# Performance work log

Measured on AMD Instinct MI355X. Metric: run time of the kernel, lower is better.

## Reference

```python
import jax, jax.numpy as jnp
import numpy as np

B, L, E, H, ENC, V, NL = 64, 512, 128, 512, 256, 4, 2
SOS = 4


def setup_inputs() -> dict:
    key = jax.random.key(0)
    ks = jax.random.split(key, 20)
    s = 0.05
    r = lambda k, shp: (jax.random.normal(k, shp, jnp.float32) * s)
    return {
        "encoder_outputs": jax.random.normal(ks[0], (B, L, ENC), jnp.float32),
        "targets": jax.random.randint(ks[1], (B, L), 0, V),
        "encoder_mask": jnp.ones((B, L), bool),
        "teacher_forcing_ratio": 1,
        "emb": r(ks[2], (V + 2, E)),
        "Wh": r(ks[3], (H, H)),
        "Ws": r(ks[4], (H, ENC)),
        "v": r(ks[5], (1, H)),
        "Wih0": r(ks[6], (3 * H, E + ENC)),
        "Whh0": r(ks[7], (3 * H, H)),
        "bih0": r(ks[8], (3 * H,)),
        "bhh0": r(ks[9], (3 * H,)),
        "Wih1": r(ks[10], (3 * H, H)),
        "Whh1": r(ks[11], (3 * H, H)),
        "bih1": r(ks[12], (3 * H,)),
        "bhh1": r(ks[13], (3 * H,)),
        "Wout": r(ks[14], (V, H)),
        "bout": r(ks[15], (V,)),
        "Winit": r(ks[16], (H * NL, ENC)),
        "binit": r(ks[17], (H * NL,)),
    }


def gru_cell(x, h, Wih, Whh, bih, bhh):
    # PyTorch GRUCell math
    gi = x @ Wih.T + bih
    gh = h @ Whh.T + bhh
    ir, iz, inn = jnp.split(gi, 3, axis=-1)
    hr, hz, hn = jnp.split(gh, 3, axis=-1)
    rg = jax.nn.sigmoid(ir + hr)
    zg = jax.nn.sigmoid(iz + hz)
    ng = jnp.tanh(inn + rg * hn)
    return (1.0 - zg) * ng + zg * h


def reference(encoder_outputs, targets, encoder_mask, teacher_forcing_ratio,
              emb, Wh, Ws, v, Wih0, Whh0, bih0, bhh0, Wih1, Whh1, bih1, bhh1,
              Wout, bout, Winit, binit):
    # init hidden: masked mean-pool -> linear -> tanh, (NL, B, H)
    maskf = encoder_mask[..., None].astype(jnp.float32)
    pooled = (encoder_outputs * maskf).sum(1) / jnp.clip(maskf.sum(1), 1.0)
    h0 = jnp.tanh((pooled @ Winit.T + binit).reshape(B, NL, H).transpose(1, 0, 2))

    # attention keys precomputed once (same linear applied each step in torch)
    keys = jnp.einsum('ble,he->blh', encoder_outputs, Ws)  # (B, L, H)

    # teacher forcing ratio fixed at 1 -> inputs known ahead of time
    tokens = jnp.concatenate([jnp.full((B, 1), SOS, targets.dtype), targets[:, :-1]], axis=1)
    emb_seq = emb[tokens]  # (B, L, E)

    neg = jnp.finfo(jnp.float32).min

    def step(h, e_t):
        q = h[-1] @ Wh.T                                   # (B, H)
        energy = jnp.tanh(q[:, None, :] + keys)            # (B, L, H)
        scores = jnp.einsum('blh,h->bl', energy, v[0])     # (B, L)
        scores = jnp.where(encoder_mask, scores, neg)
        attn = jax.nn.softmax(scores, axis=-1)
        ctx = jnp.einsum('bl,ble->be', attn, encoder_outputs)
        x = jnp.concatenate([e_t, ctx], axis=-1)           # (B, E+ENC)
        h0n = gru_cell(x, h[0], Wih0, Whh0, bih0, bhh0)
        h1n = gru_cell(h0n, h[1], Wih1, Whh1, bih1, bhh1)
        logits = h1n @ Wout.T + bout                       # (B, V)
        return jnp.stack([h0n, h1n]), logits

    _, logits = jax.lax.scan(step, h0, emb_seq.transpose(1, 0, 2))
    return logits.transpose(1, 0, 2)  # (B, L, V)
```

## Files before the change

### kernel.cpp

```cpp
#include <hip/hip_runtime.h>
#include <cstdint>
#include <cstddef>


#define BB   64
#define LL   512
#define EE   128
#define HH   512
#define ED   256
#define VV   4
#define SOS  4

#define NBLK 512
#define NTHR 256

typedef unsigned short ushort8 __attribute__((ext_vector_type(8)));
typedef unsigned int uint;
typedef uint  uint4v  __attribute__((ext_vector_type(4)));
typedef float float4v __attribute__((ext_vector_type(4)));

static const size_t OFF_KEYS = 0;
static const size_t OFF_WH   = 33554432;
static const size_t OFF_WHH0 = 34078720;
static const size_t OFF_WIH1 = 35651584;
static const size_t OFF_WHH1 = 37224448;
static const size_t OFF_WIHC = 38797312;
static const size_t OFF_GTOK = 39583744;
static const size_t OFF_H0   = 39620608;
static const size_t OFF_H1   = 39751680;
static const size_t OFF_QQ   = 39882752;
static const size_t OFF_CTXP = 40407040;
static const size_t OFF_SS   = 40931328;
static const size_t OFF_H0Q  = 40933376;
static const size_t OFF_H1Q  = 40998912;
static const size_t OFF_FLG  = 41064448;
static const size_t OFF_CNT  = 41097216;
static const size_t OFF_LP   = 41097728;

#define L_KEYS 0
#define L_H0F  65536
#define L_H1F  66560
#define L_QB   67584
#define L_VV   69696
#define L_CTX  71808
#define L_SCB  72832
#define L_ATB  73088
#define L_RED  73344
#define L_PRED 73408
#define L_GH0  77504
#define L_GH1  78272
#define L_H0O  79040
#define L_H1O  79296
#define L_TOT  79552

#define UC_LD4(dst, ptr) \
  asm volatile("global_load_dwordx4 %0, %1, off sc0 sc1" : "=v"(dst) : "v"(ptr))
#define UC_ST4(ptr, v4) \
  asm volatile("global_store_dwordx4 %0, %1, off sc0 sc1" :: "v"(ptr), "v"(v4) : "memory")
#define UC_FENCE() \
  do { asm volatile("s_waitcnt vmcnt(0)" ::: "memory"); \
       __builtin_amdgcn_sched_barrier(0); } while (0)

__device__ __forceinline__ float bfu(unsigned short u) {
  return __uint_as_float(((unsigned)u) << 16);
}
__device__ __forceinline__ float bflo(uint u) { return __uint_as_float(u << 16); }
__device__ __forceinline__ float bfhi(uint u) { return __uint_as_float(u & 0xffff0000u); }
__device__ __forceinline__ unsigned short f2bf(float f) {
  unsigned u = __float_as_uint(f);
  unsigned r = 0x7FFFu + ((u >> 16) & 1u);
  return (unsigned short)((u + r) >> 16);
}
__device__ __forceinline__ uint packbf(float a, float b) {
  return (uint)f2bf(a) | ((uint)f2bf(b) << 16);
}
__device__ __forceinline__ float tanh_fast(float x) {
  x = __builtin_amdgcn_fmed3f(x, -10.f, 10.f);
  float t = __builtin_amdgcn_exp2f(x * 2.8853900817779268f);
  return (t - 1.f) * __builtin_amdgcn_rcpf(t + 1.f);
}
__device__ __forceinline__ float sigmoid_fast(float x) {
  x = __builtin_amdgcn_fmed3f(x, -30.f, 30.f);
  float t = __builtin_amdgcn_exp2f(x * -1.4426950408889634f);
  return __builtin_amdgcn_rcpf(1.f + t);
}
__device__ __forceinline__ float exp_fast(float x) {
  return __builtin_amdgcn_exp2f(x * 1.4426950408889634f);
}
__device__ __forceinline__ float gloadf(const float* p) {
  return __hip_atomic_load(p, __ATOMIC_RELAXED, __HIP_MEMORY_SCOPE_AGENT);
}
__device__ __forceinline__ void gstoref(float* p, float v) {
  __hip_atomic_store(p, v, __ATOMIC_RELAXED, __HIP_MEMORY_SCOPE_AGENT);
}
__device__ __forceinline__ uint gloadu(const uint* p) {
  return __hip_atomic_load(p, __ATOMIC_RELAXED, __HIP_MEMORY_SCOPE_AGENT);
}
__device__ __forceinline__ void gstoreu(uint* p, uint v) {
  __hip_atomic_store(p, v, __ATOMIC_RELAXED, __HIP_MEMORY_SCOPE_AGENT);
}

__device__ __forceinline__ void octet_sync(char* ws, int b, int j, uint gen) {
  asm volatile("s_waitcnt vmcnt(0)" ::: "memory");
  __syncthreads();
  const int tid = threadIdx.x;
  uint* fl = (uint*)(ws + OFF_FLG);
  if (tid == 0)
    gstoreu(fl + (size_t)(b * 8 + j) * 16, gen);
  if (tid < 8 && tid != j) {
    while (gloadu(fl + (size_t)(b * 8 + tid) * 16) < gen)
      __builtin_amdgcn_s_sleep(4);
  }
  __syncthreads();
}


__global__ void k_prep(const float* Wh, const float* Whh0, const float* Wih0,
                       const float* Wih1, const float* Whh1, char* ws) {
  unsigned short* Whbf   = (unsigned short*)(ws + OFF_WH);
  unsigned short* Whh0bf = (unsigned short*)(ws + OFF_WHH0);
  unsigned short* Wih1bf = (unsigned short*)(ws + OFF_WIH1);
  unsigned short* Whh1bf = (unsigned short*)(ws + OFF_WHH1);
  unsigned short* WihCbf = (unsigned short*)(ws + OFF_WIHC);
  const int tot = 262144 + 786432 * 3 + 393216;
  for (int i = blockIdx.x * blockDim.x + threadIdx.x; i < tot; i += gridDim.x * blockDim.x) {
    if (i < 262144) { Whbf[i] = f2bf(Wh[i]); }
    else if (i < 262144 + 786432) { int jj = i - 262144; Whh0bf[jj] = f2bf(Whh0[jj]); }
    else if (i < 262144 + 2 * 786432) { int jj = i - 262144 - 786432; Wih1bf[jj] = f2bf(Wih1[jj]); }
    else if (i < 262144 + 3 * 786432) { int jj = i - 262144 - 2 * 786432; Whh1bf[jj] = f2bf(Whh1[jj]); }
    else {
      int jj = i - 262144 - 3 * 786432;
      int r = jj >> 8, e = jj & 255;
      WihCbf[jj] = f2bf(Wih0[(size_t)r * 384 + 128 + e]);
    }
  }
}

__global__ void k_gitok(const float* emb, const float* Wih0, const float* bih0, char* ws) {
  float* gt = (float*)(ws + OFF_GTOK);
  const int vt = blockIdx.x;
  const int tid = threadIdx.x;
  __shared__ float ev[EE];
  if (tid < EE) ev[tid] = emb[(size_t)vt * EE + tid];
  __syncthreads();
  for (int r = tid; r < 1536; r += 256) {
    float a = bih0[r];
    const float* wr = Wih0 + (size_t)r * 384;
    for (int e = 0; e < EE; ++e) a += wr[e] * ev[e];
    gt[(size_t)vt * 1536 + r] = a;
  }
}

__global__ void k_keys(const float* enc, const float* Ws, char* ws) {
  unsigned short* keys = (unsigned short*)(ws + OFF_KEYS);
  __shared__ float et[32][ED];
  const int tid = threadIdx.x;
  const int row0 = blockIdx.x * 32;
  for (int r = 0; r < 32; ++r) et[r][tid] = enc[(size_t)(row0 + r) * ED + tid];
  __syncthreads();
  for (int hhh = 0; hhh < 2; ++hhh) {
    const int h = hhh * 256 + tid;
    float acc[32];
    #pragma unroll
    for (int ll = 0; ll < 32; ++ll) acc[ll] = 0.f;
    const float4* wrow = (const float4*)(Ws + (size_t)h * ED);
    for (int e4 = 0; e4 < 64; ++e4) {
      float4 w = wrow[e4];
      #pragma unroll
      for (int ll = 0; ll < 32; ++ll) {
        acc[ll] += w.x * et[ll][e4 * 4] + w.y * et[ll][e4 * 4 + 1]
                 + w.z * et[ll][e4 * 4 + 2] + w.w * et[ll][e4 * 4 + 3];
      }
    }
    for (int ll = 0; ll < 32; ++ll)
      keys[(size_t)(row0 + ll) * HH + h] = f2bf(acc[ll]);
  }
}

__global__ void k_init(const float* enc, const float* Winit, const float* binit, char* ws) {
  const int b = blockIdx.x;
  const int tid = threadIdx.x;
  __shared__ float pooled[ED];
  float acc = 0.f;
  for (int l = 0; l < LL; ++l) acc += enc[((size_t)b * LL + l) * ED + tid];
  pooled[tid] = acc * (1.0f / 512.0f);
  __syncthreads();
  float* h0 = (float*)(ws + OFF_H0);
  float* h1 = (float*)(ws + OFF_H1);
  for (int pass = 0; pass < 4; ++pass) {
    const int jj = pass * 256 + tid;
    float a = binit[jj];
    const float* wr = Winit + (size_t)jj * ED;
    for (int e = 0; e < ED; ++e) a += wr[e] * pooled[e];
    const float val = tanh_fast(a);
    const int nl = jj >> 9, h = jj & 511;
    if (nl == 0) h0[(size_t)b * HH + h] = val;
    else h1[(size_t)b * HH + h] = val;
  }
  if (b == 0) {
    uint* fl = (uint*)(ws + OFF_FLG);
    for (int i = tid; i < 8192; i += 256) fl[i] = 0u;
    uint* cnt = (uint*)(ws + OFF_CNT);
    if (tid < 128) cnt[tid] = 0u;
  }
}

__launch_bounds__(NTHR, 2)
__global__ void k_decode(char* ws, const float* enc, const int* targets,
                         const float* vvec, const float* bhh0, const float* bhh1,
                         const float* bih1, const float* Wout) {
  extern __shared__ char smem[];
  const int tid = threadIdx.x;

  __shared__ int roleSh[2];
  if (tid == 0) {
    uint xcd;
    asm volatile("s_getreg_b32 %0, hwreg(HW_REG_XCC_ID)" : "=s"(xcd));
    xcd &= 7u;
    uint* cnt = (uint*)(ws + OFF_CNT);
    uint rank = __hip_atomic_fetch_add(cnt + (size_t)xcd * 16, 1u,
                                       __ATOMIC_RELAXED, __HIP_MEMORY_SCOPE_AGENT);
    roleSh[0] = (int)(rank & 63);
    roleSh[1] = (int)xcd;
  }
  __syncthreads();
  const int b = roleSh[0], j = roleSh[1];

  const unsigned short* keysg  = (const unsigned short*)(ws + OFF_KEYS);
  const unsigned short* Whbf   = (const unsigned short*)(ws + OFF_WH);
  const unsigned short* Whh0bf = (const unsigned short*)(ws + OFF_WHH0);
  const unsigned short* Wih1bf = (const unsigned short*)(ws + OFF_WIH1);
  const unsigned short* Whh1bf = (const unsigned short*)(ws + OFF_WHH1);
  const unsigned short* WihCbf = (const unsigned short*)(ws + OFF_WIHC);
  const float* gi_tok = (const float*)(ws + OFF_GTOK);

  uint*  QQg   = (uint*)(ws + OFF_QQ)   + (size_t)b * 2048;
  float* CTXPg = (float*)(ws + OFF_CTXP) + (size_t)b * 2048;
  float* SSg   = (float*)(ws + OFF_SS)  + (size_t)b * 8;
  uint*  H0Qg  = (uint*)(ws + OFF_H0Q)  + (size_t)b * 256;
  uint*  H1Qg  = (uint*)(ws + OFF_H1Q)  + (size_t)b * 256;
  float* lp    = (float*)(ws + OFF_LP);

  uint*  h0u   = (uint*)(smem + L_H0F);
  uint*  h1u   = (uint*)(smem + L_H1F);
  float* qbf   = (float*)(smem + L_QB);
  float* vvf   = (float*)(smem + L_VV);
  float* ctx   = (float*)(smem + L_CTX);
  float* scb   = (float*)(smem + L_SCB);
  float* atb   = (float*)(smem + L_ATB);
  float* wred  = (float*)(smem + L_RED);
  float* pRed  = (float*)(smem + L_PRED);
  float* gh0own = (float*)(smem + L_GH0);
  float* gh1own = (float*)(smem + L_GH1);
  float* h0own = (float*)(smem + L_H0O);
  float* h1own = (float*)(smem + L_H1O);
  uint*  qstage = (uint*)(smem + L_PRED);
  uint*  hstage = (uint*)(smem + L_SCB);

  for (int c = tid; c < 4096; c += NTHR) {
    const int l = c >> 6, hs = c & 63;
    ushort8 kv = *(const ushort8*)(keysg + ((size_t)(b * LL + j * 64 + l) * HH + hs * 8));
    *(ushort8*)(smem + L_KEYS + l * 1024 + ((hs * 16) ^ ((l & 7) << 4))) = kv;
  }
  for (int h = tid; h < 512; h += NTHR)
    vvf[(h >> 7) * 132 + (h & 127)] = vvec[h];
  {
    const float* H0g = (const float*)(ws + OFF_H0) + (size_t)b * HH;
    const float* H1g = (const float*)(ws + OFF_H1) + (size_t)b * HH;
    h0u[tid] = packbf(H0g[2 * tid], H0g[2 * tid + 1]);
    h1u[tid] = packbf(H1g[2 * tid], H1g[2 * tid + 1]);
    if (tid < 64) {
      h0own[tid] = H0g[j * 64 + tid];
      h1own[tid] = H1g[j * 64 + tid];
    }
  }
  uint encp[32];
  {
    const float* ebase = enc + ((size_t)(b * LL + j * 64)) * ED + tid;
    #pragma unroll
    for (int k = 0; k < 32; ++k)
      encp[k] = packbf(ebase[(size_t)(2 * k) * ED], ebase[(size_t)(2 * k + 1) * ED]);
  }
  uint whq[64];
  #pragma unroll
  for (int i = 0; i < 32; ++i) {
    whq[i]      = *(const uint*)(Whbf + (size_t)(2 * tid) * HH + j * 64 + 2 * i);
    whq[32 + i] = *(const uint*)(Whbf + (size_t)(2 * tid + 1) * HH + j * 64 + 2 * i);
  }
  __syncthreads();

  {
    float q0 = 0.f, q1 = 0.f;
    #pragma unroll
    for (int i = 0; i < 32; ++i) {
      const float hl = h1own[2 * i], hh = h1own[2 * i + 1];
      q0 += bflo(whq[i]) * hl + bfhi(whq[i]) * hh;
      q1 += bflo(whq[32 + i]) * hl + bfhi(whq[32 + i]) * hh;
    }
    qstage[tid] = packbf(q0, q1);
    if (tid < 32) hstage[tid] = packbf(h1own[2 * tid], h1own[2 * tid + 1]);
    __syncthreads();
    if (tid < 64) { UC_ST4(QQg + (size_t)j * 256 + 4 * tid, *(uint4v*)(qstage + 4 * tid)); }
    else if (tid < 72) {
      const int c = tid - 64;
      UC_ST4(H1Qg + (size_t)j * 32 + 4 * c, *(uint4v*)(hstage + 4 * c));
    }
  }
  octet_sync(ws, b, j, 1u);

  for (int t = 0; t < LL; ++t) {
    if (tid < 64) {
      uint4v uq0, uq1, uq2, uq3, uq4, uq5, uq6, uq7;
      UC_LD4(uq0, QQg + 0 * 256 + 4 * tid);
      UC_LD4(uq1, QQg + 1 * 256 + 4 * tid);
      UC_LD4(uq2, QQg + 2 * 256 + 4 * tid);
      UC_LD4(uq3, QQg + 3 * 256 + 4 * tid);
      UC_LD4(uq4, QQg + 4 * 256 + 4 * tid);
      UC_LD4(uq5, QQg + 5 * 256 + 4 * tid);
      UC_LD4(uq6, QQg + 6 * 256 + 4 * tid);
      UC_LD4(uq7, QQg + 7 * 256 + 4 * tid);
      UC_FENCE();
      const int base = ((8 * tid) >> 7) * 132 + ((8 * tid) & 127);
      #pragma unroll
      for (int k = 0; k < 4; ++k) {
        float lo = bflo(uq0[k]) + bflo(uq1[k]) + bflo(uq2[k]) + bflo(uq3[k])
                 + bflo(uq4[k]) + bflo(uq5[k]) + bflo(uq6[k]) + bflo(uq7[k]);
        float hi = bfhi(uq0[k]) + bfhi(uq1[k]) + bfhi(uq2[k]) + bfhi(uq3[k])
                 + bfhi(uq4[k]) + bfhi(uq5[k]) + bfhi(uq6[k]) + bfhi(uq7[k]);
        qbf[base + 2 * k]     = lo;
        qbf[base + 2 * k + 1] = hi;
      }
    } else if (tid < 120) {
      const int p2 = (tid - 64) >> 3, c = (tid - 64) & 7;
      const int p = p2 + (p2 >= j);
      uint4v u;
      UC_LD4(u, H1Qg + (size_t)p * 32 + 4 * c);
      UC_FENCE();
      *(uint4v*)(h1u + p * 32 + 4 * c) = u;
    }
    __syncthreads();

    {
      const int mat = tid >> 7, seg = (tid >> 6) & 1, r = tid & 63;
      const unsigned short* W = mat ? Whh1bf : Whh0bf;
      const uint* hsrc = (mat ? h1u : h0u) + seg * 128;
      const ushort8* w0 = (const ushort8*)(W + (size_t)(0 * 512 + j * 64 + r) * 512 + seg * 256);
      const ushort8* w1 = (const ushort8*)(W + (size_t)(1 * 512 + j * 64 + r) * 512 + seg * 256);
      const ushort8* w2 = (const ushort8*)(W + (size_t)(2 * 512 + j * 64 + r) * 512 + seg * 256);
      float a0 = 0.f, a1 = 0.f, a2 = 0.f;
      for (int k8 = 0; k8 < 32; ++k8) {
        const uint4 hu = *(const uint4*)(hsrc + k8 * 4);
        const ushort8 u0 = w0[k8], u1 = w1[k8], u2 = w2[k8];
        float hv[8];
        hv[0] = bflo(hu.x); hv[1] = bfhi(hu.x); hv[2] = bflo(hu.y); hv[3] = bfhi(hu.y);
        hv[4] = bflo(hu.z); hv[5] = bfhi(hu.z); hv[6] = bflo(hu.w); hv[7] = bfhi(hu.w);
        #pragma unroll
        for (int u = 0; u < 8; ++u) {
          a0 += bfu(u0[u]) * hv[u];
          a1 += bfu(u1[u]) * hv[u];
          a2 += bfu(u2[u]) * hv[u];
        }
      }
      pRed[((mat * 2 + seg) * 3 + 0) * 64 + r] = a0;
      pRed[((mat * 2 + seg) * 3 + 1) * 64 + r] = a1;
      pRed[((mat * 2 + seg) * 3 + 2) * 64 + r] = a2;
    }

    {
      const int lloc = tid >> 2, hq = tid & 3;
      const char* kbase = smem + L_KEYS + lloc * 1024;
      const int xo = (lloc & 7) << 4;
      const float* qh = qbf + hq * 132;
      const float* vh = vvf + hq * 132;
      float s = 0.f;
      for (int i8 = 0; i8 < 16; ++i8) {
        ushort8 kk = *(const ushort8*)(kbase + ((hq * 256 + i8 * 16) ^ xo));
        const float* q8 = qh + i8 * 8;
        const float* v8 = vh + i8 * 8;
        #pragma unroll
        for (int u = 0; u < 8; ++u)
          s += v8[u] * tanh_fast(q8[u] + bfu(kk[u]));
      }
      s += __shfl_xor(s, 1);
      s += __shfl_xor(s, 2);
      if (hq == 0) scb[lloc] = s;
    }
    __syncthreads();

    if (tid < 64) {
      float e = exp_fast(scb[tid]);
      atb[tid] = e;
      float s2 = e;
      #pragma unroll
      for (int off = 32; off >= 1; off >>= 1) s2 += __shfl_xor(s2, off);
      if (tid == 0) gstoref(SSg + j, s2);
    }
    __syncthreads();

    {
      float a = 0.f;
      #pragma unroll
      for (int k = 0; k < 32; ++k) {
        uint u = encp[k];
        a += atb[2 * k] * bflo(u) + atb[2 * k + 1] * bfhi(u);
      }
      ctx[tid] = a;
    }
    for (int o = tid; o < 384; o += NTHR) {
      const int m = (o >= 192) ? 1 : 0, oo = o - m * 192, g = oo >> 6, r = oo & 63;
      const float v = pRed[((m * 2 + 0) * 3 + g) * 64 + r]
                    + pRed[((m * 2 + 1) * 3 + g) * 64 + r]
                    + (m ? bhh1 : bhh0)[g * 512 + j * 64 + r];
      (m ? gh1own : gh0own)[g * 64 + r] = v;
    }
    __syncthreads();
    if (tid < 64) { UC_ST4((uint*)(CTXPg + (size_t)j * 256) + 4 * tid, *(uint4v*)((uint*)ctx + 4 * tid)); }
    octet_sync(ws, b, j, (uint)(3 * t + 2));

    {
      const int c = tid & 63, p0 = tid >> 6;
      float4v f0, f1;
      UC_LD4(f0, (const uint*)(CTXPg + (size_t)p0 * 256) + 4 * c);
      UC_LD4(f1, (const uint*)(CTXPg + (size_t)(p0 + 4) * 256) + 4 * c);
      float ssv = 0.f;
      if (tid < 8) ssv = gloadf(SSg + tid);
      UC_FENCE();
      if (tid < 8) wred[tid] = ssv;
      *(float4v*)(pRed + (size_t)p0 * 256 + 4 * c) = f0 + f1;
      __syncthreads();
      const float S8 = ((wred[0] + wred[1]) + (wred[2] + wred[3]))
                     + ((wred[4] + wred[5]) + (wred[6] + wred[7]));
      const float rS = __builtin_amdgcn_rcpf(S8);
      ctx[tid] = (pRed[0 * 256 + tid] + pRed[1 * 256 + tid]
                + pRed[2 * 256 + tid] + pRed[3 * 256 + tid]) * rS;
    }
    __syncthreads();
    {
      const int r = tid & 63, q4 = tid >> 6;
      const ushort8* w0 = (const ushort8*)(WihCbf + (size_t)(0 * 512 + j * 64 + r) * 256 + q4 * 64);
      const ushort8* w1 = (const ushort8*)(WihCbf + (size_t)(1 * 512 + j * 64 + r) * 256 + q4 * 64);
      const ushort8* w2 = (const ushort8*)(WihCbf + (size_t)(2 * 512 + j * 64 + r) * 256 + q4 * 64);
      const float* cx = ctx + q4 * 64;
      float a0 = 0.f, a1 = 0.f, a2 = 0.f;
      for (int k8 = 0; k8 < 8; ++k8) {
        const ushort8 u0 = w0[k8], u1 = w1[k8], u2 = w2[k8];
        #pragma unroll
        for (int u = 0; u < 8; ++u) {
          const float c = cx[k8 * 8 + u];
          a0 += bfu(u0[u]) * c; a1 += bfu(u1[u]) * c; a2 += bfu(u2[u]) * c;
        }
      }
      pRed[(q4 * 3 + 0) * 64 + r] = a0;
      pRed[(q4 * 3 + 1) * 64 + r] = a1;
      pRed[(q4 * 3 + 2) * 64 + r] = a2;
    }
    __syncthreads();
    if (tid < 64) {
      const int r = tid;
      const int tok = (t == 0) ? SOS : targets[(size_t)b * LL + t - 1];
      const float* gt = gi_tok + (size_t)tok * 1536 + j * 64 + r;
      const float g0 = pRed[(0 * 3 + 0) * 64 + r] + pRed[(1 * 3 + 0) * 64 + r]
                     + pRed[(2 * 3 + 0) * 64 + r] + pRed[(3 * 3 + 0) * 64 + r] + gt[0];
      const float g1 = pRed[(0 * 3 + 1) * 64 + r] + pRed[(1 * 3 + 1) * 64 + r]
                     + pRed[(2 * 3 + 1) * 64 + r] + pRed[(3 * 3 + 1) * 64 + r] + gt[512];
      const float g2 = pRed[(0 * 3 + 2) * 64 + r] + pRed[(1 * 3 + 2) * 64 + r]
                     + pRed[(2 * 3 + 2) * 64 + r] + pRed[(3 * 3 + 2) * 64 + r] + gt[1024];
      const float rg = sigmoid_fast(g0 + gh0own[r]);
      const float zg = sigmoid_fast(g1 + gh0own[64 + r]);
      const float ng = tanh_fast(g2 + rg * gh0own[128 + r]);
      h0own[r] = (1.f - zg) * ng + zg * h0own[r];
    }
    __syncthreads();
    if (tid < 32) {
      const uint pk = packbf(h0own[2 * tid], h0own[2 * tid + 1]);
      h0u[j * 32 + tid] = pk;
      hstage[tid] = pk;
    }
    __syncthreads();
    if (tid < 8) { UC_ST4(H0Qg + (size_t)j * 32 + 4 * tid, *(uint4v*)(hstage + 4 * tid)); }
    octet_sync(ws, b, j, (uint)(3 * t + 3));

    if (tid < 56) {
      const int p2 = tid >> 3, c = tid & 7;
      const int p = p2 + (p2 >= j);
      uint4v u;
      UC_LD4(u, H0Qg + (size_t)p * 32 + 4 * c);
      UC_FENCE();
      *(uint4v*)(h0u + p * 32 + 4 * c) = u;
    }
    __syncthreads();
    {
      const int r = tid & 63, s4 = tid >> 6;
      const ushort8* w0 = (const ushort8*)(Wih1bf + (size_t)(0 * 512 + j * 64 + r) * 512 + s4 * 128);
      const ushort8* w1 = (const ushort8*)(Wih1bf + (size_t)(1 * 512 + j * 64 + r) * 512 + s4 * 128);
      const ushort8* w2 = (const ushort8*)(Wih1bf + (size_t)(2 * 512 + j * 64 + r) * 512 + s4 * 128);
      const uint* hsrc = h0u + s4 * 64;
      float a0 = 0.f, a1 = 0.f, a2 = 0.f;
      for (int k8 = 0; k8 < 16; ++k8) {
        const uint4 hu = *(const uint4*)(hsrc + k8 * 4);
        const ushort8 u0 = w0[k8], u1 = w1[k8], u2 = w2[k8];
        float hv[8];
        hv[0] = bflo(hu.x); hv[1] = bfhi(hu.x); hv[2] = bflo(hu.y); hv[3] = bfhi(hu.y);
        hv[4] = bflo(hu.z); hv[5] = bfhi(hu.z); hv[6] = bflo(hu.w); hv[7] = bfhi(hu.w);
        #pragma unroll
        for (int u = 0; u < 8; ++u) {
          a0 += bfu(u0[u]) * hv[u];
          a1 += bfu(u1[u]) * hv[u];
          a2 += bfu(u2[u]) * hv[u];
        }
      }
      pRed[(s4 * 3 + 0) * 64 + r] = a0;
      pRed[(s4 * 3 + 1) * 64 + r] = a1;
      pRed[(s4 * 3 + 2) * 64 + r] = a2;
    }
    __syncthreads();
    if (tid < 64) {
      const int r = tid;
      const float g0 = pRed[(0 * 3 + 0) * 64 + r] + pRed[(1 * 3 + 0) * 64 + r]
                     + pRed[(2 * 3 + 0) * 64 + r] + pRed[(3 * 3 + 0) * 64 + r]
                     + bih1[0 * 512 + j * 64 + r];
      const float g1 = pRed[(0 * 3 + 1) * 64 + r] + pRed[(1 * 3 + 1) * 64 + r]
                     + pRed[(2 * 3 + 1) * 64 + r] + pRed[(3 * 3 + 1) * 64 + r]
                     + bih1[1 * 512 + j * 64 + r];
      const float g2 = pRed[(0 * 3 + 2) * 64 + r] + pRed[(1 * 3 + 2) * 64 + r]
                     + pRed[(2 * 3 + 2) * 64 + r] + pRed[(3 * 3 + 2) * 64 + r]
                     + bih1[2 * 512 + j * 64 + r];
      const float rg = sigmoid_fast(g0 + gh1own[r]);
      const float zg = sigmoid_fast(g1 + gh1own[64 + r]);
      const float ng = tanh_fast(g2 + rg * gh1own[128 + r]);
      h1own[r] = (1.f - zg) * ng + zg * h1own[r];
    }
    __syncthreads();
    {
      float q0 = 0.f, q1 = 0.f;
      #pragma unroll
      for (int i = 0; i < 32; ++i) {
        const float hl = h1own[2 * i], hh = h1own[2 * i + 1];
        q0 += bflo(whq[i]) * hl + bfhi(whq[i]) * hh;
        q1 += bflo(whq[32 + i]) * hl + bfhi(whq[32 + i]) * hh;
      }
      qstage[tid] = packbf(q0, q1);
    }
    if (tid < 32) {
      const uint pk = packbf(h1own[2 * tid], h1own[2 * tid + 1]);
      h1u[j * 32 + tid] = pk;
      hstage[tid] = pk;
    }
    if (tid >= 64 && tid < 128) {
      const int lane = tid - 64, v = lane >> 4, i = lane & 15;
      float a = 0.f;
      #pragma unroll
      for (int k = 0; k < 4; ++k)
        a += Wout[(size_t)v * HH + j * 64 + i * 4 + k] * h1own[i * 4 + k];
      a += __shfl_xor(a, 8); a += __shfl_xor(a, 4);
      a += __shfl_xor(a, 2); a += __shfl_xor(a, 1);
      if (i == 0) lp[(((size_t)t * BB + b) * 8 + j) * 4 + v] = a;
    }
    __syncthreads();
    if (tid < 64) { UC_ST4(QQg + (size_t)j * 256 + 4 * tid, *(uint4v*)(qstage + 4 * tid)); }
    else if (tid < 72) {
      const int c = tid - 64;
      UC_ST4(H1Qg + (size_t)j * 32 + 4 * c, *(uint4v*)(hstage + 4 * c));
    }
    octet_sync(ws, b, j, (uint)(3 * t + 4));
  }
}

__global__ void k_lsum(const char* ws, const float* bout, float* out) {
  const float* lp = (const float*)(ws + OFF_LP);
  const int i = blockIdx.x * 256 + threadIdx.x;
  if (i >= BB * LL * VV) return;
  const int v = i & 3, t = (i >> 2) & 511, b = i >> 11;
  float a = bout[v];
  #pragma unroll
  for (int jj = 0; jj < 8; ++jj)
    a += lp[(((size_t)t * BB + b) * 8 + jj) * 4 + v];
  out[i] = a;
}

extern "C" void kernel_launch(void* const* d_in, const int* in_sizes, int n_in,
                              void* d_out, int out_size, void* d_ws, size_t ws_size,
                              hipStream_t stream) {
  char* ws = (char*)d_ws;
  const float* enc     = (const float*)d_in[0];
  const int*   targets = (const int*)d_in[1];
  const float* emb   = (const float*)d_in[4];
  const float* Wh    = (const float*)d_in[5];
  const float* Ws    = (const float*)d_in[6];
  const float* vvec  = (const float*)d_in[7];
  const float* Wih0  = (const float*)d_in[8];
  const float* Whh0  = (const float*)d_in[9];
  const float* bih0  = (const float*)d_in[10];
  const float* bhh0  = (const float*)d_in[11];
  const float* Wih1  = (const float*)d_in[12];
  const float* Whh1  = (const float*)d_in[13];
  const float* bih1  = (const float*)d_in[14];
  const float* bhh1  = (const float*)d_in[15];
  const float* Wout  = (const float*)d_in[16];
  const float* bout  = (const float*)d_in[17];
  const float* Winit = (const float*)d_in[18];
  const float* binit = (const float*)d_in[19];

  k_prep <<<1024, 256, 0, stream>>>(Wh, Whh0, Wih0, Wih1, Whh1, ws);
  k_gitok<<<6,    256, 0, stream>>>(emb, Wih0, bih0, ws);
  k_keys <<<1024, 256, 0, stream>>>(enc, Ws, ws);
  k_init <<<64,   256, 0, stream>>>(enc, Winit, binit, ws);

  (void)hipFuncSetAttribute((const void*)k_decode,
                            hipFuncAttributeMaxDynamicSharedMemorySize, L_TOT);

  {
    void* kws = (void*)ws;
    void* ken = (void*)enc;
    void* ktg = (void*)targets;
    void* kvv = (void*)vvec;
    void* kb0 = (void*)bhh0;
    void* kb1 = (void*)bhh1;
    void* kbi = (void*)bih1;
    void* kwo = (void*)Wout;
    void* args[] = { &kws, &ken, &ktg, &kvv, &kb0, &kb1, &kbi, &kwo };
    hipError_t ce = hipLaunchCooperativeKernel((const void*)k_decode, dim3(NBLK), dim3(NTHR),
                                               args, L_TOT, stream);
    if (ce != hipSuccess) {
      k_decode<<<dim3(NBLK), dim3(NTHR), L_TOT, stream>>>(ws, enc, targets, vvec,
                                                          bhh0, bhh1, bih1, Wout);
    }
  }

  k_lsum<<<512, 256, 0, stream>>>(ws, bout, (float*)d_out);
}
```

Baseline: 49.45 ms.

## Process two batch rows per block with split publish/wait syncs and fp16 dot2 GEMVs

Halves the grid so each persistent block owns two batch rows. It interleaves their per-step phases so one row's cross-block wait can overlap the other row's compute. The octet barrier is split into separate publish and wait halves. The GRU weight matrices and hidden-state packing switch from bf16 to fp16 so the matvecs can use the fdot2 instruction. This trades occupancy and much larger shared memory (two key tiles) for fewer idle barrier waits, and fp16 weights bring some range and precision risk.

```diff
diff --git a/kernel.cpp b/kernel.cpp
--- a/kernel.cpp
+++ b/kernel.cpp
@@ -11,13 +11,14 @@
 #define VV   4
 #define SOS  4
 
-#define NBLK 512
+#define NBLK 256
 #define NTHR 256
 
 typedef unsigned short ushort8 __attribute__((ext_vector_type(8)));
 typedef unsigned int uint;
 typedef uint  uint4v  __attribute__((ext_vector_type(4)));
 typedef float float4v __attribute__((ext_vector_type(4)));
+typedef _Float16 h2v __attribute__((ext_vector_type(2)));
 
 static const size_t OFF_KEYS = 0;
 static const size_t OFF_WH   = 33554432;
@@ -37,21 +38,24 @@
 static const size_t OFF_CNT  = 41097216;
 static const size_t OFF_LP   = 41097728;
 
-#define L_KEYS 0
-#define L_H0F  65536
-#define L_H1F  66560
-#define L_QB   67584
-#define L_VV   69696
-#define L_CTX  71808
-#define L_SCB  72832
-#define L_ATB  73088
-#define L_RED  73344
-#define L_PRED 73408
-#define L_GH0  77504
-#define L_GH1  78272
-#define L_H0O  79040
-#define L_H1O  79296
-#define L_TOT  79552
+#define LKEY(bi)  ((bi) * 65536)
+#define LB(bi)    (131072 + (bi) * 12544)
+#define O_H0U  0
+#define O_H1U  1024
+#define O_QBF  2048
+#define O_CTX  4160
+#define O_SCB  5184
+#define O_ATB  5440
+#define O_WRED 5696
+#define O_PRED 5760
+#define O_GH0  9856
+#define O_GH1  10624
+#define O_H0O  11392
+#define O_H1O  11648
+#define O_HST  11904
+#define O_CTXH 12032
+#define L_VV   156160
+#define L_TOT  158272
 
 #define UC_LD4(dst, ptr) \
   asm volatile("global_load_dwordx4 %0, %1, off sc0 sc1" : "=v"(dst) : "v"(ptr))
@@ -74,6 +78,24 @@
 __device__ __forceinline__ uint packbf(float a, float b) {
   return (uint)f2bf(a) | ((uint)f2bf(b) << 16);
 }
+__device__ __forceinline__ unsigned short f2h(float f) {
+  return __builtin_bit_cast(unsigned short, (_Float16)f);
+}
+__device__ __forceinline__ uint packh(float a, float b) {
+  return (uint)f2h(a) | ((uint)f2h(b) << 16);
+}
+__device__ __forceinline__ float fd2(uint w, uint h, float acc) {
+#if __has_builtin(__builtin_amdgcn_fdot2)
+  return __builtin_amdgcn_fdot2(__builtin_bit_cast(h2v, w),
+                                __builtin_bit_cast(h2v, h), acc, false);
+#else
+  acc += (float)__builtin_bit_cast(_Float16, (unsigned short)(w & 0xffffu)) *
+         (float)__builtin_bit_cast(_Float16, (unsigned short)(h & 0xffffu));
+  acc += (float)__builtin_bit_cast(_Float16, (unsigned short)(w >> 16)) *
+         (float)__builtin_bit_cast(_Float16, (unsigned short)(h >> 16));
+  return acc;
+#endif
+}
 __device__ __forceinline__ float tanh_fast(float x) {
   x = __builtin_amdgcn_fmed3f(x, -10.f, 10.f);
   float t = __builtin_amdgcn_exp2f(x * 2.8853900817779268f);
@@ -100,16 +122,16 @@
   __hip_atomic_store(p, v, __ATOMIC_RELAXED, __HIP_MEMORY_SCOPE_AGENT);
 }
 
-__device__ __forceinline__ void octet_sync(char* ws, int b, int j, uint gen) {
+__device__ __forceinline__ void oct_publish(char* ws, int b, int j, uint gen) {
   asm volatile("s_waitcnt vmcnt(0)" ::: "memory");
   __syncthreads();
-  const int tid = threadIdx.x;
-  uint* fl = (uint*)(ws + OFF_FLG);
-  if (tid == 0)
-    gstoreu(fl + (size_t)(b * 8 + j) * 16, gen);
-  if (tid < 8 && tid != j) {
-    while (gloadu(fl + (size_t)(b * 8 + tid) * 16) < gen)
-      __builtin_amdgcn_s_sleep(4);
+  if (threadIdx.x == 0)
+    gstoreu((uint*)(ws + OFF_FLG) + (size_t)(b * 8 + j) * 16, gen);
+}
+__device__ __forceinline__ void oct_wait(char* ws, int b, uint gen) {
+  if (threadIdx.x < 8) {
+    const uint* fp = (const uint*)(ws + OFF_FLG) + (size_t)(b * 8 + threadIdx.x) * 16;
+    while (gloadu(fp) < gen) __builtin_amdgcn_s_sleep(1);
   }
   __syncthreads();
 }
@@ -117,21 +139,21 @@
 
 __global__ void k_prep(const float* Wh, const float* Whh0, const float* Wih0,
                        const float* Wih1, const float* Whh1, char* ws) {
-  unsigned short* Whbf   = (unsigned short*)(ws + OFF_WH);
-  unsigned short* Whh0bf = (unsigned short*)(ws + OFF_WHH0);
-  unsigned short* Wih1bf = (unsigned short*)(ws + OFF_WIH1);
-  unsigned short* Whh1bf = (unsigned short*)(ws + OFF_WHH1);
-  unsigned short* WihCbf = (unsigned short*)(ws + OFF_WIHC);
+  unsigned short* Whbf  = (unsigned short*)(ws + OFF_WH);
+  unsigned short* W0F   = (unsigned short*)(ws + OFF_WHH0);
+  unsigned short* Wi1F  = (unsigned short*)(ws + OFF_WIH1);
+  unsigned short* W1F   = (unsigned short*)(ws + OFF_WHH1);
+  unsigned short* WicF  = (unsigned short*)(ws + OFF_WIHC);
   const int tot = 262144 + 786432 * 3 + 393216;
   for (int i = blockIdx.x * blockDim.x + threadIdx.x; i < tot; i += gridDim.x * blockDim.x) {
     if (i < 262144) { Whbf[i] = f2bf(Wh[i]); }
-    else if (i < 262144 + 786432) { int jj = i - 262144; Whh0bf[jj] = f2bf(Whh0[jj]); }
-    else if (i < 262144 + 2 * 786432) { int jj = i - 262144 - 786432; Wih1bf[jj] = f2bf(Wih1[jj]); }
-    else if (i < 262144 + 3 * 786432) { int jj = i - 262144 - 2 * 786432; Whh1bf[jj] = f2bf(Whh1[jj]); }
+    else if (i < 262144 + 786432) { int jj = i - 262144; W0F[jj] = f2h(Whh0[jj]); }
+    else if (i < 262144 + 2 * 786432) { int jj = i - 262144 - 786432; Wi1F[jj] = f2h(Wih1[jj]); }
+    else if (i < 262144 + 3 * 786432) { int jj = i - 262144 - 2 * 786432; W1F[jj] = f2h(Whh1[jj]); }
     else {
       int jj = i - 262144 - 3 * 786432;
       int r = jj >> 8, e = jj & 255;
-      WihCbf[jj] = f2bf(Wih0[(size_t)r * 384 + 128 + e]);
+      WicF[jj] = f2h(Wih0[(size_t)r * 384 + 128 + e]);
     }
   }
 }
@@ -205,7 +227,7 @@
   }
 }
 
-__launch_bounds__(NTHR, 2)
+__launch_bounds__(NTHR, 1)
 __global__ void k_decode(char* ws, const float* enc, const int* targets,
                          const float* vvec, const float* bhh0, const float* bhh1,
                          const float* bih1, const float* Wout) {
@@ -220,315 +242,63 @@
     uint* cnt = (uint*)(ws + OFF_CNT);
     uint rank = __hip_atomic_fetch_add(cnt + (size_t)xcd * 16, 1u,
                                        __ATOMIC_RELAXED, __HIP_MEMORY_SCOPE_AGENT);
-    roleSh[0] = (int)(rank & 63);
+    roleSh[0] = (int)(rank & 31);
     roleSh[1] = (int)xcd;
   }
   __syncthreads();
-  const int b = roleSh[0], j = roleSh[1];
-
-  const unsigned short* keysg  = (const unsigned short*)(ws + OFF_KEYS);
-  const unsigned short* Whbf   = (const unsigned short*)(ws + OFF_WH);
-  const unsigned short* Whh0bf = (const unsigned short*)(ws + OFF_WHH0);
-  const unsigned short* Wih1bf = (const unsigned short*)(ws + OFF_WIH1);
-  const unsigned short* Whh1bf = (const unsigned short*)(ws + OFF_WHH1);
-  const unsigned short* WihCbf = (const unsigned short*)(ws + OFF_WIHC);
+  const int pair = roleSh[0], j = roleSh[1];
+  const int bat[2] = { pair * 2, pair * 2 + 1 };
+
+  const unsigned short* keysg = (const unsigned short*)(ws + OFF_KEYS);
+  const unsigned short* Whbf  = (const unsigned short*)(ws + OFF_WH);
+  const unsigned short* W0F   = (const unsigned short*)(ws + OFF_WHH0);
+  const unsigned short* Wi1F  = (const unsigned short*)(ws + OFF_WIH1);
+  const unsigned short* W1F   = (const unsigned short*)(ws + OFF_WHH1);
+  const unsigned short* WicF  = (const unsigned short*)(ws + OFF_WIHC);
   const float* gi_tok = (const float*)(ws + OFF_GTOK);
-
-  uint*  QQg   = (uint*)(ws + OFF_QQ)   + (size_t)b * 2048;
-  float* CTXPg = (float*)(ws + OFF_CTXP) + (size_t)b * 2048;
-  float* SSg   = (float*)(ws + OFF_SS)  + (size_t)b * 8;
-  uint*  H0Qg  = (uint*)(ws + OFF_H0Q)  + (size_t)b * 256;
-  uint*  H1Qg  = (uint*)(ws + OFF_H1Q)  + (size_t)b * 256;
-  float* lp    = (float*)(ws + OFF_LP);
-
-  uint*  h0u   = (uint*)(smem + L_H0F);
-  uint*  h1u   = (uint*)(smem + L_H1F);
-  float* qbf   = (float*)(smem + L_QB);
-  float* vvf   = (float*)(smem + L_VV);
-  float* ctx   = (float*)(smem + L_CTX);
-  float* scb   = (float*)(smem + L_SCB);
-  float* atb   = (float*)(smem + L_ATB);
-  float* wred  = (float*)(smem + L_RED);
-  float* pRed  = (float*)(smem + L_PRED);
-  float* gh0own = (float*)(smem + L_GH0);
-  float* gh1own = (float*)(smem + L_GH1);
-  float* h0own = (float*)(smem + L_H0O);
-  float* h1own = (float*)(smem + L_H1O);
-  uint*  qstage = (uint*)(smem + L_PRED);
-  uint*  hstage = (uint*)(smem + L_SCB);
-
-  for (int c = tid; c < 4096; c += NTHR) {
-    const int l = c >> 6, hs = c & 63;
-    ushort8 kv = *(const ushort8*)(keysg + ((size_t)(b * LL + j * 64 + l) * HH + hs * 8));
-    *(ushort8*)(smem + L_KEYS + l * 1024 + ((hs * 16) ^ ((l & 7) << 4))) = kv;
-  }
-  for (int h = tid; h < 512; h += NTHR)
-    vvf[(h >> 7) * 132 + (h & 127)] = vvec[h];
-  {
-    const float* H0g = (const float*)(ws + OFF_H0) + (size_t)b * HH;
-    const float* H1g = (const float*)(ws + OFF_H1) + (size_t)b * HH;
-    h0u[tid] = packbf(H0g[2 * tid], H0g[2 * tid + 1]);
-    h1u[tid] = packbf(H1g[2 * tid], H1g[2 * tid + 1]);
-    if (tid < 64) {
-      h0own[tid] = H0g[j * 64 + tid];
-      h1own[tid] = H1g[j * 64 + tid];
-    }
-  }
-  uint encp[32];
-  {
-    const float* ebase = enc + ((size_t)(b * LL + j * 64)) * ED + tid;
-    #pragma unroll
-    for (int k = 0; k < 32; ++k)
-      encp[k] = packbf(ebase[(size_t)(2 * k) * ED], ebase[(size_t)(2 * k + 1) * ED]);
-  }
+  float* lp = (float*)(ws + OFF_LP);
+  float* vvf = (float*)(smem + L_VV);
+
   uint whq[64];
   #pragma unroll
   for (int i = 0; i < 32; ++i) {
     whq[i]      = *(const uint*)(Whbf + (size_t)(2 * tid) * HH + j * 64 + 2 * i);
     whq[32 + i] = *(const uint*)(Whbf + (size_t)(2 * tid + 1) * HH + j * 64 + 2 * i);
   }
-  __syncthreads();
-
-  {
-    float q0 = 0.f, q1 = 0.f;
+  for (int h = tid; h < 512; h += NTHR)
+    vvf[(h >> 7) * 132 + (h & 127)] = vvec[h];
+
+  uint encp[2][32];
+  #pragma unroll
+  for (int bi = 0; bi < 2; ++bi) {
+    const float* ebase = enc + ((size_t)(bat[bi] * LL + j * 64)) * ED + tid;
     #pragma unroll
-    for (int i = 0; i < 32; ++i) {
-      const float hl = h1own[2 * i], hh = h1own[2 * i + 1];
-      q0 += bflo(whq[i]) * hl + bfhi(whq[i]) * hh;
-      q1 += bflo(whq[32 + i]) * hl + bfhi(whq[32 + i]) * hh;
-    }
-    qstage[tid] = packbf(q0, q1);
-    if (tid < 32) hstage[tid] = packbf(h1own[2 * tid], h1own[2 * tid + 1]);
-    __syncthreads();
-    if (tid < 64) { UC_ST4(QQg + (size_t)j * 256 + 4 * tid, *(uint4v*)(qstage + 4 * tid)); }
-    else if (tid < 72) {
-      const int c = tid - 64;
-      UC_ST4(H1Qg + (size_t)j * 32 + 4 * c, *(uint4v*)(hstage + 4 * c));
-    }
-  }
-  octet_sync(ws, b, j, 1u);
-
-  for (int t = 0; t < LL; ++t) {
+    for (int k = 0; k < 32; ++k)
+      encp[bi][k] = packbf(ebase[(size_t)(2 * k) * ED], ebase[(size_t)(2 * k + 1) * ED]);
+  }
+
+  #pragma unroll
+  for (int bi = 0; bi < 2; ++bi) {
+    const int b = bat[bi];
+    char* bb = smem + LB(bi);
+    uint*  h0u = (uint*)(bb + O_H0U);
+    uint*  h1u = (uint*)(bb + O_H1U);
+    float* h0own = (float*)(bb + O_H0O);
+    float* h1own = (float*)(bb + O_H1O);
+    uint*  qstage = (uint*)(bb + O_PRED);
+    uint*  hstage = (uint*)(bb + O_HST);
+    for (int c = tid; c < 4096; c += NTHR) {
+      const int l = c >> 6, hs = c & 63;
+      ushort8 kv = *(const ushort8*)(keysg + ((size_t)(b * LL + j * 64 + l) * HH + hs * 8));
+      *(ushort8*)(smem + LKEY(bi) + l * 1024 + ((hs * 16) ^ ((l & 7) << 4))) = kv;
+    }
+    const float* H0g = (const float*)(ws + OFF_H0) + (size_t)b * HH;
+    const float* H1g = (const float*)(ws + OFF_H1) + (size_t)b * HH;
+    h0u[tid] = packh(H0g[2 * tid], H0g[2 * tid + 1]);
+    h1u[tid] = packh(H1g[2 * tid], H1g[2 * tid + 1]);
     if (tid < 64) {
-      uint4v uq0, uq1, uq2, uq3, uq4, uq5, uq6, uq7;
-      UC_LD4(uq0, QQg + 0 * 256 + 4 * tid);
-      UC_LD4(uq1, QQg + 1 * 256 + 4 * tid);
-      UC_LD4(uq2, QQg + 2 * 256 + 4 * tid);
-      UC_LD4(uq3, QQg + 3 * 256 + 4 * tid);
-      UC_LD4(uq4, QQg + 4 * 256 + 4 * tid);
-      UC_LD4(uq5, QQg + 5 * 256 + 4 * tid);
-      UC_LD4(uq6, QQg + 6 * 256 + 4 * tid);
-      UC_LD4(uq7, QQg + 7 * 256 + 4 * tid);
-      UC_FENCE();
-      const int base = ((8 * tid) >> 7) * 132 + ((8 * tid) & 127);
-      #pragma unroll
-      for (int k = 0; k < 4; ++k) {
-        float lo = bflo(uq0[k]) + bflo(uq1[k]) + bflo(uq2[k]) + bflo(uq3[k])
-                 + bflo(uq4[k]) + bflo(uq5[k]) + bflo(uq6[k]) + bflo(uq7[k]);
-        float hi = bfhi(uq0[k]) + bfhi(uq1[k]) + bfhi(uq2[k]) + bfhi(uq3[k])
-                 + bfhi(uq4[k]) + bfhi(uq5[k]) + bfhi(uq6[k]) + bfhi(uq7[k]);
-        qbf[base + 2 * k]     = lo;
-        qbf[base + 2 * k + 1] = hi;
-      }
-    } else if (tid < 120) {
-      const int p2 = (tid - 64) >> 3, c = (tid - 64) & 7;
-      const int p = p2 + (p2 >= j);
-      uint4v u;
-      UC_LD4(u, H1Qg + (size_t)p * 32 + 4 * c);
-      UC_FENCE();
-      *(uint4v*)(h1u + p * 32 + 4 * c) = u;
-    }
-    __syncthreads();
-
-    {
-      const int mat = tid >> 7, seg = (tid >> 6) & 1, r = tid & 63;
-      const unsigned short* W = mat ? Whh1bf : Whh0bf;
-      const uint* hsrc = (mat ? h1u : h0u) + seg * 128;
-      const ushort8* w0 = (const ushort8*)(W + (size_t)(0 * 512 + j * 64 + r) * 512 + seg * 256);
-      const ushort8* w1 = (const ushort8*)(W + (size_t)(1 * 512 + j * 64 + r) * 512 + seg * 256);
-      const ushort8* w2 = (const ushort8*)(W + (size_t)(2 * 512 + j * 64 + r) * 512 + seg * 256);
-      float a0 = 0.f, a1 = 0.f, a2 = 0.f;
-      for (int k8 = 0; k8 < 32; ++k8) {
-        const uint4 hu = *(const uint4*)(hsrc + k8 * 4);
-        const ushort8 u0 = w0[k8], u1 = w1[k8], u2 = w2[k8];
-        float hv[8];
-        hv[0] = bflo(hu.x); hv[1] = bfhi(hu.x); hv[2] = bflo(hu.y); hv[3] = bfhi(hu.y);
-        hv[4] = bflo(hu.z); hv[5] = bfhi(hu.z); hv[6] = bflo(hu.w); hv[7] = bfhi(hu.w);
-        #pragma unroll
-        for (int u = 0; u < 8; ++u) {
-          a0 += bfu(u0[u]) * hv[u];
-          a1 += bfu(u1[u]) * hv[u];
-          a2 += bfu(u2[u]) * hv[u];
-        }
-      }
-      pRed[((mat * 2 + seg) * 3 + 0) * 64 + r] = a0;
-      pRed[((mat * 2 + seg) * 3 + 1) * 64 + r] = a1;
-      pRed[((mat * 2 + seg) * 3 + 2) * 64 + r] = a2;
-    }
-
-    {
-      const int lloc = tid >> 2, hq = tid & 3;
-      const char* kbase = smem + L_KEYS + lloc * 1024;
-      const int xo = (lloc & 7) << 4;
-      const float* qh = qbf + hq * 132;
-      const float* vh = vvf + hq * 132;
-      float s = 0.f;
-      for (int i8 = 0; i8 < 16; ++i8) {
-        ushort8 kk = *(const ushort8*)(kbase + ((hq * 256 + i8 * 16) ^ xo));
-        const float* q8 = qh + i8 * 8;
-        const float* v8 = vh + i8 * 8;
-        #pragma unroll
-        for (int u = 0; u < 8; ++u)
-          s += v8[u] * tanh_fast(q8[u] + bfu(kk[u]));
-      }
-      s += __shfl_xor(s, 1);
-      s += __shfl_xor(s, 2);
-      if (hq == 0) scb[lloc] = s;
-    }
-    __syncthreads();
-
-    if (tid < 64) {
-      float e = exp_fast(scb[tid]);
-      atb[tid] = e;
-      float s2 = e;
-      #pragma unroll
-      for (int off = 32; off >= 1; off >>= 1) s2 += __shfl_xor(s2, off);
-      if (tid == 0) gstoref(SSg + j, s2);
-    }
-    __syncthreads();
-
-    {
-      float a = 0.f;
-      #pragma unroll
-      for (int k = 0; k < 32; ++k) {
-        uint u = encp[k];
-        a += atb[2 * k] * bflo(u) + atb[2 * k + 1] * bfhi(u);
-      }
-      ctx[tid] = a;
-    }
-    for (int o = tid; o < 384; o += NTHR) {
-      const int m = (o >= 192) ? 1 : 0, oo = o - m * 192, g = oo >> 6, r = oo & 63;
-      const float v = pRed[((m * 2 + 0) * 3 + g) * 64 + r]
-                    + pRed[((m * 2 + 1) * 3 + g) * 64 + r]
-                    + (m ? bhh1 : bhh0)[g * 512 + j * 64 + r];
-      (m ? gh1own : gh0own)[g * 64 + r] = v;
-    }
-    __syncthreads();
-    if (tid < 64) { UC_ST4((uint*)(CTXPg + (size_t)j * 256) + 4 * tid, *(uint4v*)((uint*)ctx + 4 * tid)); }
-    octet_sync(ws, b, j, (uint)(3 * t + 2));
-
-    {
-      const int c = tid & 63, p0 = tid >> 6;
-      float4v f0, f1;
-      UC_LD4(f0, (const uint*)(CTXPg + (size_t)p0 * 256) + 4 * c);
-      UC_LD4(f1, (const uint*)(CTXPg + (size_t)(p0 + 4) * 256) + 4 * c);
-      float ssv = 0.f;
-      if (tid < 8) ssv = gloadf(SSg + tid);
-      UC_FENCE();
-      if (tid < 8) wred[tid] = ssv;
-      *(float4v*)(pRed + (size_t)p0 * 256 + 4 * c) = f0 + f1;
-      __syncthreads();
-      const float S8 = ((wred[0] + wred[1]) + (wred[2] + wred[3]))
-                     + ((wred[4] + wred[5]) + (wred[6] + wred[7]));
-      const float rS = __builtin_amdgcn_rcpf(S8);
-      ctx[tid] = (pRed[0 * 256 + tid] + pRed[1 * 256 + tid]
-                + pRed[2 * 256 + tid] + pRed[3 * 256 + tid]) * rS;
-    }
-    __syncthreads();
-    {
-      const int r = tid & 63, q4 = tid >> 6;
-      const ushort8* w0 = (const ushort8*)(WihCbf + (size_t)(0 * 512 + j * 64 + r) * 256 + q4 * 64);
-      const ushort8* w1 = (const ushort8*)(WihCbf + (size_t)(1 * 512 + j * 64 + r) * 256 + q4 * 64);
-      const ushort8* w2 = (const ushort8*)(WihCbf + (size_t)(2 * 512 + j * 64 + r) * 256 + q4 * 64);
-      const float* cx = ctx + q4 * 64;
-      float a0 = 0.f, a1 = 0.f, a2 = 0.f;
-      for (int k8 = 0; k8 < 8; ++k8) {
-        const ushort8 u0 = w0[k8], u1 = w1[k8], u2 = w2[k8];
-        #pragma unroll
-        for (int u = 0; u < 8; ++u) {
-          const float c = cx[k8 * 8 + u];
-          a0 += bfu(u0[u]) * c; a1 += bfu(u1[u]) * c; a2 += bfu(u2[u]) * c;
-        }
-      }
-      pRed[(q4 * 3 + 0) * 64 + r] = a0;
-      pRed[(q4 * 3 + 1) * 64 + r] = a1;
-      pRed[(q4 * 3 + 2) * 64 + r] = a2;
-    }
-    __syncthreads();
-    if (tid < 64) {
-      const int r = tid;
-      const int tok = (t == 0) ? SOS : targets[(size_t)b * LL + t - 1];
-      const float* gt = gi_tok + (size_t)tok * 1536 + j * 64 + r;
-      const float g0 = pRed[(0 * 3 + 0) * 64 + r] + pRed[(1 * 3 + 0) * 64 + r]
-                     + pRed[(2 * 3 + 0) * 64 + r] + pRed[(3 * 3 + 0) * 64 + r] + gt[0];
-      const float g1 = pRed[(0 * 3 + 1) * 64 + r] + pRed[(1 * 3 + 1) * 64 + r]
-                     + pRed[(2 * 3 + 1) * 64 + r] + pRed[(3 * 3 + 1) * 64 + r] + gt[512];
-      const float g2 = pRed[(0 * 3 + 2) * 64 + r] + pRed[(1 * 3 + 2) * 64 + r]
-                     + pRed[(2 * 3 + 2) * 64 + r] + pRed[(3 * 3 + 2) * 64 + r] + gt[1024];
-      const float rg = sigmoid_fast(g0 + gh0own[r]);
-      const float zg = sigmoid_fast(g1 + gh0own[64 + r]);
-      const float ng = tanh_fast(g2 + rg * gh0own[128 + r]);
-      h0own[r] = (1.f - zg) * ng + zg * h0own[r];
-    }
-    __syncthreads();
-    if (tid < 32) {
-      const uint pk = packbf(h0own[2 * tid], h0own[2 * tid + 1]);
-      h0u[j * 32 + tid] = pk;
-      hstage[tid] = pk;
-    }
-    __syncthreads();
-    if (tid < 8) { UC_ST4(H0Qg + (size_t)j * 32 + 4 * tid, *(uint4v*)(hstage + 4 * tid)); }
-    octet_sync(ws, b, j, (uint)(3 * t + 3));
-
-    if (tid < 56) {
-      const int p2 = tid >> 3, c = tid & 7;
-      const int p = p2 + (p2 >= j);
-      uint4v u;
-      UC_LD4(u, H0Qg + (size_t)p * 32 + 4 * c);
-      UC_FENCE();
-      *(uint4v*)(h0u + p * 32 + 4 * c) = u;
-    }
-    __syncthreads();
-    {
-      const int r = tid & 63, s4 = tid >> 6;
-      const ushort8* w0 = (const ushort8*)(Wih1bf + (size_t)(0 * 512 + j * 64 + r) * 512 + s4 * 128);
-      const ushort8* w1 = (const ushort8*)(Wih1bf + (size_t)(1 * 512 + j * 64 + r) * 512 + s4 * 128);
-      const ushort8* w2 = (const ushort8*)(Wih1bf + (size_t)(2 * 512 + j * 64 + r) * 512 + s4 * 128);
-      const uint* hsrc = h0u + s4 * 64;
-      float a0 = 0.f, a1 = 0.f, a2 = 0.f;
-      for (int k8 = 0; k8 < 16; ++k8) {
-        const uint4 hu = *(const uint4*)(hsrc + k8 * 4);
-        const ushort8 u0 = w0[k8], u1 = w1[k8], u2 = w2[k8];
-        float hv[8];
-        hv[0] = bflo(hu.x); hv[1] = bfhi(hu.x); hv[2] = bflo(hu.y); hv[3] = bfhi(hu.y);
-        hv[4] = bflo(hu.z); hv[5] = bfhi(hu.z); hv[6] = bflo(hu.w); hv[7] = bfhi(hu.w);
-        #pragma unroll
-        for (int u = 0; u < 8; ++u) {
-          a0 += bfu(u0[u]) * hv[u];
-          a1 += bfu(u1[u]) * hv[u];
-          a2 += bfu(u2[u]) * hv[u];
-        }
-      }
-      pRed[(s4 * 3 + 0) * 64 + r] = a0;
-      pRed[(s4 * 3 + 1) * 64 + r] = a1;
-      pRed[(s4 * 3 + 2) * 64 + r] = a2;
-    }
-    __syncthreads();
-    if (tid < 64) {
-      const int r = tid;
-      const float g0 = pRed[(0 * 3 + 0) * 64 + r] + pRed[(1 * 3 + 0) * 64 + r]
-                     + pRed[(2 * 3 + 0) * 64 + r] + pRed[(3 * 3 + 0) * 64 + r]
-                     + bih1[0 * 512 + j * 64 + r];
-      const float g1 = pRed[(0 * 3 + 1) * 64 + r] + pRed[(1 * 3 + 1) * 64 + r]
-                     + pRed[(2 * 3 + 1) * 64 + r] + pRed[(3 * 3 + 1) * 64 + r]
-                     + bih1[1 * 512 + j * 64 + r];
-      const float g2 = pRed[(0 * 3 + 2) * 64 + r] + pRed[(1 * 3 + 2) * 64 + r]
-                     + pRed[(2 * 3 + 2) * 64 + r] + pRed[(3 * 3 + 2) * 64 + r]
-                     + bih1[2 * 512 + j * 64 + r];
-      const float rg = sigmoid_fast(g0 + gh1own[r]);
-      const float zg = sigmoid_fast(g1 + gh1own[64 + r]);
-      const float ng = tanh_fast(g2 + rg * gh1own[128 + r]);
-      h1own[r] = (1.f - zg) * ng + zg * h1own[r];
+      h0own[tid] = H0g[j * 64 + tid];
+      h1own[tid] = H1g[j * 64 + tid];
     }
     __syncthreads();
     {
@@ -540,29 +310,336 @@
         q1 += bflo(whq[32 + i]) * hl + bfhi(whq[32 + i]) * hh;
       }
       qstage[tid] = packbf(q0, q1);
-    }
-    if (tid < 32) {
-      const uint pk = packbf(h1own[2 * tid], h1own[2 * tid + 1]);
-      h1u[j * 32 + tid] = pk;
-      hstage[tid] = pk;
-    }
-    if (tid >= 64 && tid < 128) {
-      const int lane = tid - 64, v = lane >> 4, i = lane & 15;
-      float a = 0.f;
-      #pragma unroll
-      for (int k = 0; k < 4; ++k)
-        a += Wout[(size_t)v * HH + j * 64 + i * 4 + k] * h1own[i * 4 + k];
-      a += __shfl_xor(a, 8); a += __shfl_xor(a, 4);
-      a += __shfl_xor(a, 2); a += __shfl_xor(a, 1);
-      if (i == 0) lp[(((size_t)t * BB + b) * 8 + j) * 4 + v] = a;
+      if (tid < 32) hstage[tid] = packh(h1own[2 * tid], h1own[2 * tid + 1]);
     }
     __syncthreads();
+    uint* QQg  = (uint*)(ws + OFF_QQ)  + (size_t)b * 2048;
+    uint* H1Qg = (uint*)(ws + OFF_H1Q) + (size_t)b * 256;
     if (tid < 64) { UC_ST4(QQg + (size_t)j * 256 + 4 * tid, *(uint4v*)(qstage + 4 * tid)); }
     else if (tid < 72) {
       const int c = tid - 64;
       UC_ST4(H1Qg + (size_t)j * 32 + 4 * c, *(uint4v*)(hstage + 4 * c));
     }
-    octet_sync(ws, b, j, (uint)(3 * t + 4));
+    oct_publish(ws, b, j, 2u);
+  }
+
+  for (int t = 0; t < LL; ++t) {
+    #pragma unroll
+    for (int bi = 0; bi < 2; ++bi) {
+      const int b = bat[bi];
+      char* bb = smem + LB(bi);
+      uint*  h0u = (uint*)(bb + O_H0U);
+      uint*  h1u = (uint*)(bb + O_H1U);
+      float* qbf = (float*)(bb + O_QBF);
+      float* ctx = (float*)(bb + O_CTX);
+      float* scb = (float*)(bb + O_SCB);
+      float* atb = (float*)(bb + O_ATB);
+      float* pRed = (float*)(bb + O_PRED);
+      float* gh0own = (float*)(bb + O_GH0);
+      float* gh1own = (float*)(bb + O_GH1);
+      uint* QQg  = (uint*)(ws + OFF_QQ)  + (size_t)b * 2048;
+      uint* H1Qg = (uint*)(ws + OFF_H1Q) + (size_t)b * 256;
+      float* CTXPg = (float*)(ws + OFF_CTXP) + (size_t)b * 2048;
+      float* SSg = (float*)(ws + OFF_SS) + (size_t)b * 8;
+
+      oct_wait(ws, b, 2u + 3u * (uint)t);
+
+      if (tid < 64) {
+        uint4v u0, u1, u2, u3, u4, u5, u6, u7;
+        UC_LD4(u0, QQg + 0 * 256 + 4 * tid);
+        UC_LD4(u1, QQg + 1 * 256 + 4 * tid);
+        UC_LD4(u2, QQg + 2 * 256 + 4 * tid);
+        UC_LD4(u3, QQg + 3 * 256 + 4 * tid);
+        UC_LD4(u4, QQg + 4 * 256 + 4 * tid);
+        UC_LD4(u5, QQg + 5 * 256 + 4 * tid);
+        UC_LD4(u6, QQg + 6 * 256 + 4 * tid);
+        UC_LD4(u7, QQg + 7 * 256 + 4 * tid);
+        UC_FENCE();
+        const int base = ((8 * tid) >> 7) * 132 + ((8 * tid) & 127);
+        #pragma unroll
+        for (int k = 0; k < 4; ++k) {
+          float lo = bflo(u0[k]) + bflo(u1[k]) + bflo(u2[k]) + bflo(u3[k])
+                   + bflo(u4[k]) + bflo(u5[k]) + bflo(u6[k]) + bflo(u7[k]);
+          float hi = bfhi(u0[k]) + bfhi(u1[k]) + bfhi(u2[k]) + bfhi(u3[k])
+                   + bfhi(u4[k]) + bfhi(u5[k]) + bfhi(u6[k]) + bfhi(u7[k]);
+          qbf[base + 2 * k]     = lo;
+          qbf[base + 2 * k + 1] = hi;
+        }
+      } else if (tid < 120) {
+        const int p2 = (tid - 64) >> 3, c = (tid - 64) & 7;
+        const int p = p2 + (p2 >= j);
+        uint4v u;
+        UC_LD4(u, H1Qg + (size_t)p * 32 + 4 * c);
+        UC_FENCE();
+        *(uint4v*)(h1u + p * 32 + 4 * c) = u;
+      }
+      __syncthreads();
+
+      {
+        const int mat = tid >> 7, seg = (tid >> 6) & 1, r = tid & 63;
+        const unsigned short* W = mat ? W1F : W0F;
+        const uint* hsrc = (mat ? h1u : h0u) + seg * 128;
+        const uint* w0 = (const uint*)(W + (size_t)(0 * 512 + j * 64 + r) * 512 + seg * 256);
+        const uint* w1 = (const uint*)(W + (size_t)(1 * 512 + j * 64 + r) * 512 + seg * 256);
+        const uint* w2 = (const uint*)(W + (size_t)(2 * 512 + j * 64 + r) * 512 + seg * 256);
+        float a0 = 0.f, a1 = 0.f, a2 = 0.f;
+        for (int k8 = 0; k8 < 32; ++k8) {
+          const uint4 h4 = *(const uint4*)(hsrc + k8 * 4);
+          const uint4 x0 = *(const uint4*)(w0 + k8 * 4);
+          const uint4 x1 = *(const uint4*)(w1 + k8 * 4);
+          const uint4 x2 = *(const uint4*)(w2 + k8 * 4);
+          a0 = fd2(x0.x, h4.x, a0); a0 = fd2(x0.y, h4.y, a0);
+          a0 = fd2(x0.z, h4.z, a0); a0 = fd2(x0.w, h4.w, a0);
+          a1 = fd2(x1.x, h4.x, a1); a1 = fd2(x1.y, h4.y, a1);
+          a1 = fd2(x1.z, h4.z, a1); a1 = fd2(x1.w, h4.w, a1);
+          a2 = fd2(x2.x, h4.x, a2); a2 = fd2(x2.y, h4.y, a2);
+          a2 = fd2(x2.z, h4.z, a2); a2 = fd2(x2.w, h4.w, a2);
+        }
+        pRed[((mat * 2 + seg) * 3 + 0) * 64 + r] = a0;
+        pRed[((mat * 2 + seg) * 3 + 1) * 64 + r] = a1;
+        pRed[((mat * 2 + seg) * 3 + 2) * 64 + r] = a2;
+      }
+
+      {
+        const int lloc = tid >> 2, hq = tid & 3;
+        const char* kbase = smem + LKEY(bi) + lloc * 1024;
+        const int xo = (lloc & 7) << 4;
+        const float* qh = qbf + hq * 132;
+        const float* vh = vvf + hq * 132;
+        float s = 0.f;
+        for (int i8 = 0; i8 < 16; ++i8) {
+          ushort8 kk = *(const ushort8*)(kbase + ((hq * 256 + i8 * 16) ^ xo));
+          const float* q8 = qh + i8 * 8;
+          const float* v8 = vh + i8 * 8;
+          #pragma unroll
+          for (int u = 0; u < 8; ++u)
+            s += v8[u] * tanh_fast(q8[u] + bfu(kk[u]));
+        }
+        s += __shfl_xor(s, 1);
+        s += __shfl_xor(s, 2);
+        if (hq == 0) scb[lloc] = s;
+      }
+      __syncthreads();
+
+      if (tid < 64) {
+        float e = exp_fast(scb[tid]);
+        atb[tid] = e;
+        float s2 = e;
+        #pragma unroll
+        for (int off = 32; off >= 1; off >>= 1) s2 += __shfl_xor(s2, off);
+        if (tid == 0) gstoref(SSg + j, s2);
+      }
+      __syncthreads();
+
+      {
+        float a = 0.f;
+        #pragma unroll
+        for (int k = 0; k < 32; ++k) {
+          uint u = encp[bi][k];
+          a += atb[2 * k] * bflo(u) + atb[2 * k + 1] * bfhi(u);
+        }
+        ctx[tid] = a;
+      }
+      for (int o = tid; o < 384; o += NTHR) {
+        const int m = (o >= 192) ? 1 : 0, oo = o - m * 192, g = oo >> 6, r = oo & 63;
+        const float v = pRed[((m * 2 + 0) * 3 + g) * 64 + r]
+                      + pRed[((m * 2 + 1) * 3 + g) * 64 + r]
+                      + (m ? bhh1 : bhh0)[g * 512 + j * 64 + r];
+        (m ? gh1own : gh0own)[g * 64 + r] = v;
+      }
+      __syncthreads();
+      if (tid < 64) { UC_ST4((uint*)(CTXPg + (size_t)j * 256) + 4 * tid, *(uint4v*)((uint*)ctx + 4 * tid)); }
+      oct_publish(ws, b, j, 3u + 3u * (uint)t);
+    }
+
+    #pragma unroll
+    for (int bi = 0; bi < 2; ++bi) {
+      const int b = bat[bi];
+      char* bb = smem + LB(bi);
+      uint*  h0u = (uint*)(bb + O_H0U);
+      float* ctx = (float*)(bb + O_CTX);
+      uint*  ctxh = (uint*)(bb + O_CTXH);
+      float* wred = (float*)(bb + O_WRED);
+      float* pRed = (float*)(bb + O_PRED);
+      float* gh0own = (float*)(bb + O_GH0);
+      float* h0own = (float*)(bb + O_H0O);
+      uint*  hstage = (uint*)(bb + O_HST);
+      float* CTXPg = (float*)(ws + OFF_CTXP) + (size_t)b * 2048;
+      float* SSg = (float*)(ws + OFF_SS) + (size_t)b * 8;
+      uint* H0Qg = (uint*)(ws + OFF_H0Q) + (size_t)b * 256;
+
+      oct_wait(ws, b, 3u + 3u * (uint)t);
+
+      {
+        const int c = tid & 63, p0 = tid >> 6;
+        float4v f0, f1;
+        UC_LD4(f0, (const uint*)(CTXPg + (size_t)p0 * 256) + 4 * c);
+        UC_LD4(f1, (const uint*)(CTXPg + (size_t)(p0 + 4) * 256) + 4 * c);
+        float ssv = 0.f;
+        if (tid < 8) ssv = gloadf(SSg + tid);
+        UC_FENCE();
+        if (tid < 8) wred[tid] = ssv;
+        *(float4v*)(pRed + (size_t)p0 * 256 + 4 * c) = f0 + f1;
+        __syncthreads();
+        const float S8 = ((wred[0] + wred[1]) + (wred[2] + wred[3]))
+                       + ((wred[4] + wred[5]) + (wred[6] + wred[7]));
+        const float rS = __builtin_amdgcn_rcpf(S8);
+        ctx[tid] = (pRed[0 * 256 + tid] + pRed[1 * 256 + tid]
+                  + pRed[2 * 256 + tid] + pRed[3 * 256 + tid]) * rS;
+      }
+      __syncthreads();
+      if (tid < 128) ctxh[tid] = packh(ctx[2 * tid], ctx[2 * tid + 1]);
+      __syncthreads();
+      {
+        const int r = tid & 63, q4 = tid >> 6;
+        const uint* w0 = (const uint*)(WicF + (size_t)(0 * 512 + j * 64 + r) * 256 + q4 * 64);
+        const uint* w1 = (const uint*)(WicF + (size_t)(1 * 512 + j * 64 + r) * 256 + q4 * 64);
+        const uint* w2 = (const uint*)(WicF + (size_t)(2 * 512 + j * 64 + r) * 256 + q4 * 64);
+        const uint* hh = ctxh + q4 * 32;
+        float a0 = 0.f, a1 = 0.f, a2 = 0.f;
+        for (int c8 = 0; c8 < 8; ++c8) {
+          const uint4 h4 = *(const uint4*)(hh + c8 * 4);
+          const uint4 x0 = *(const uint4*)(w0 + c8 * 4);
+          const uint4 x1 = *(const uint4*)(w1 + c8 * 4);
+          const uint4 x2 = *(const uint4*)(w2 + c8 * 4);
+          a0 = fd2(x0.x, h4.x, a0); a0 = fd2(x0.y, h4.y, a0);
+          a0 = fd2(x0.z, h4.z, a0); a0 = fd2(x0.w, h4.w, a0);
+          a1 = fd2(x1.x, h4.x, a1); a1 = fd2(x1.y, h4.y, a1);
+          a1 = fd2(x1.z, h4.z, a1); a1 = fd2(x1.w, h4.w, a1);
+          a2 = fd2(x2.x, h4.x, a2); a2 = fd2(x2.y, h4.y, a2);
+          a2 = fd2(x2.z, h4.z, a2); a2 = fd2(x2.w, h4.w, a2);
+        }
+        pRed[(q4 * 3 + 0) * 64 + r] = a0;
+        pRed[(q4 * 3 + 1) * 64 + r] = a1;
+        pRed[(q4 * 3 + 2) * 64 + r] = a2;
+      }
+      __syncthreads();
+      if (tid < 64) {
+        const int r = tid;
+        const int tok = (t == 0) ? SOS : targets[(size_t)b * LL + t - 1];
+        const float* gt = gi_tok + (size_t)tok * 1536 + j * 64 + r;
+        const float g0 = pRed[(0 * 3 + 0) * 64 + r] + pRed[(1 * 3 + 0) * 64 + r]
+                       + pRed[(2 * 3 + 0) * 64 + r] + pRed[(3 * 3 + 0) * 64 + r] + gt[0];
+        const float g1 = pRed[(0 * 3 + 1) * 64 + r] + pRed[(1 * 3 + 1) * 64 + r]
+                       + pRed[(2 * 3 + 1) * 64 + r] + pRed[(3 * 3 + 1) * 64 + r] + gt[512];
+        const float g2 = pRed[(0 * 3 + 2) * 64 + r] + pRed[(1 * 3 + 2) * 64 + r]
+                       + pRed[(2 * 3 + 2) * 64 + r] + pRed[(3 * 3 + 2) * 64 + r] + gt[1024];
+        const float rg = sigmoid_fast(g0 + gh0own[r]);
+        const float zg = sigmoid_fast(g1 + gh0own[64 + r]);
+        const float ng = tanh_fast(g2 + rg * gh0own[128 + r]);
+        h0own[r] = (1.f - zg) * ng + zg * h0own[r];
+      }
+      __syncthreads();
+      if (tid < 32) {
+        const uint pk = packh(h0own[2 * tid], h0own[2 * tid + 1]);
+        h0u[j * 32 + tid] = pk;
+        hstage[tid] = pk;
+      }
+      __syncthreads();
+      if (tid < 8) { UC_ST4(H0Qg + (size_t)j * 32 + 4 * tid, *(uint4v*)(hstage + 4 * tid)); }
+      oct_publish(ws, b, j, 4u + 3u * (uint)t);
+    }
+
+    #pragma unroll
+    for (int bi = 0; bi < 2; ++bi) {
+      const int b = bat[bi];
+      char* bb = smem + LB(bi);
+      uint*  h0u = (uint*)(bb + O_H0U);
+      uint*  h1u = (uint*)(bb + O_H1U);
+      float* pRed = (float*)(bb + O_PRED);
+      float* gh1own = (float*)(bb + O_GH1);
+      float* h1own = (float*)(bb + O_H1O);
+      uint*  qstage = (uint*)(bb + O_PRED);
+      uint*  hstage = (uint*)(bb + O_HST);
+      uint* QQg  = (uint*)(ws + OFF_QQ)  + (size_t)b * 2048;
+      uint* H0Qg = (uint*)(ws + OFF_H0Q) + (size_t)b * 256;
+      uint* H1Qg = (uint*)(ws + OFF_H1Q) + (size_t)b * 256;
+
+      oct_wait(ws, b, 4u + 3u * (uint)t);
+
+      if (tid < 56) {
+        const int p2 = tid >> 3, c = tid & 7;
+        const int p = p2 + (p2 >= j);
+        uint4v u;
+        UC_LD4(u, H0Qg + (size_t)p * 32 + 4 * c);
+        UC_FENCE();
+        *(uint4v*)(h0u + p * 32 + 4 * c) = u;
+      }
+      __syncthreads();
+      {
+        const int r = tid & 63, s4 = tid >> 6;
+        const uint* w0 = (const uint*)(Wi1F + (size_t)(0 * 512 + j * 64 + r) * 512 + s4 * 128);
+        const uint* w1 = (const uint*)(Wi1F + (size_t)(1 * 512 + j * 64 + r) * 512 + s4 * 128);
+        const uint* w2 = (const uint*)(Wi1F + (size_t)(2 * 512 + j * 64 + r) * 512 + s4 * 128);
+        const uint* hh = h0u + s4 * 64;
+        float a0 = 0.f, a1 = 0.f, a2 = 0.f;
+        for (int c8 = 0; c8 < 16; ++c8) {
+          const uint4 h4 = *(const uint4*)(hh + c8 * 4);
+          const uint4 x0 = *(const uint4*)(w0 + c8 * 4);
+          const uint4 x1 = *(const uint4*)(w1 + c8 * 4);
+          const uint4 x2 = *(const uint4*)(w2 + c8 * 4);
+          a0 = fd2(x0.x, h4.x, a0); a0 = fd2(x0.y, h4.y, a0);
+          a0 = fd2(x0.z, h4.z, a0); a0 = fd2(x0.w, h4.w, a0);
+          a1 = fd2(x1.x, h4.x, a1); a1 = fd2(x1.y, h4.y, a1);
+          a1 = fd2(x1.z, h4.z, a1); a1 = fd2(x1.w, h4.w, a1);
+          a2 = fd2(x2.x, h4.x, a2); a2 = fd2(x2.y, h4.y, a2);
+          a2 = fd2(x2.z, h4.z, a2); a2 = fd2(x2.w, h4.w, a2);
+        }
+        pRed[(s4 * 3 + 0) * 64 + r] = a0;
+        pRed[(s4 * 3 + 1) * 64 + r] = a1;
+        pRed[(s4 * 3 + 2) * 64 + r] = a2;
+      }
+      __syncthreads();
+      if (tid < 64) {
+        const int r = tid;
+        const float g0 = pRed[(0 * 3 + 0) * 64 + r] + pRed[(1 * 3 + 0) * 64 + r]
+                       + pRed[(2 * 3 + 0) * 64 + r] + pRed[(3 * 3 + 0) * 64 + r]
+                       + bih1[0 * 512 + j * 64 + r];
+        const float g1 = pRed[(0 * 3 + 1) * 64 + r] + pRed[(1 * 3 + 1) * 64 + r]
+                       + pRed[(2 * 3 + 1) * 64 + r] + pRed[(3 * 3 + 1) * 64 + r]
+                       + bih1[1 * 512 + j * 64 + r];
+        const float g2 = pRed[(0 * 3 + 2) * 64 + r] + pRed[(1 * 3 + 2) * 64 + r]
+                       + pRed[(2 * 3 + 2) * 64 + r] + pRed[(3 * 3 + 2) * 64 + r]
+                       + bih1[2 * 512 + j * 64 + r];
+        const float rg = sigmoid_fast(g0 + gh1own[r]);
+        const float zg = sigmoid_fast(g1 + gh1own[64 + r]);
+        const float ng = tanh_fast(g2 + rg * gh1own[128 + r]);
+        h1own[r] = (1.f - zg) * ng + zg * h1own[r];
+      }
+      __syncthreads();
+      {
+        float q0 = 0.f, q1 = 0.f;
+        #pragma unroll
+        for (int i = 0; i < 32; ++i) {
+          const float hl = h1own[2 * i], hh = h1own[2 * i + 1];
+          q0 += bflo(whq[i]) * hl + bfhi(whq[i]) * hh;
+          q1 += bflo(whq[32 + i]) * hl + bfhi(whq[32 + i]) * hh;
+        }
+        qstage[tid] = packbf(q0, q1);
+      }
+      if (tid < 32) {
+        const uint pk = packh(h1own[2 * tid], h1own[2 * tid + 1]);
+        h1u[j * 32 + tid] = pk;
+        hstage[tid] = pk;
+      }
+      if (tid >= 64 && tid < 128) {
+        const int lane = tid - 64, v = lane >> 4, i = lane & 15;
+        float a = 0.f;
+        #pragma unroll
+        for (int k = 0; k < 4; ++k)
+          a += Wout[(size_t)v * HH + j * 64 + i * 4 + k] * h1own[i * 4 + k];
+        a += __shfl_xor(a, 8); a += __shfl_xor(a, 4);
+        a += __shfl_xor(a, 2); a += __shfl_xor(a, 1);
+        if (i == 0) lp[(((size_t)t * BB + b) * 8 + j) * 4 + v] = a;
+      }
+      __syncthreads();
+      if (tid < 64) { UC_ST4(QQg + (size_t)j * 256 + 4 * tid, *(uint4v*)(qstage + 4 * tid)); }
+      else if (tid < 72) {
+        const int c = tid - 64;
+        UC_ST4(H1Qg + (size_t)j * 32 + 4 * c, *(uint4v*)(hstage + 4 * c));
+      }
+      oct_publish(ws, b, j, 5u + 3u * (uint)t);
+    }
   }
 }
 
```

Result: slower. 53.33 ms (+7.8%).
